# Optimization experiments

Hardware: AMD Instinct MI355X
Metric: run time of the kernel (lower is better)

Reference implementation:

```python
import jax, jax.numpy as jnp
import numpy as np

B, I, O, E = 4096, 256, 256, 8


def setup_inputs() -> dict:
    key = jax.random.key(0)
    k1, k2, k3 = jax.random.split(key, 3)
    return {
        "x": jax.random.normal(k1, (B, I), jnp.float32),
        "W": jax.random.normal(k2, (E, I, O), jnp.float32) * (1.0 / np.sqrt(I)),
        "Wp": jax.random.normal(k3, (E, I), jnp.float32) * (1.0 / np.sqrt(I)),
        "bp": jnp.zeros((E,), jnp.float32),
    }


def reference(x, W, Wp, bp):
    # Router: nn.Linear(in, E) -> sigmoid -> hard one-hot on argmax (BinarySoftActivation)
    g = jax.nn.sigmoid(x @ Wp.T + bp)                              # [B, E]
    onehot = (g == g.max(axis=1, keepdims=True)).astype(g.dtype)   # [B, E] (multi-hot on ties, as in torch)
    gate = g + jax.lax.stop_gradient(onehot - g)                   # straight-through estimator
    # Original: weight[b] = sum_e gate[b,e] * W[e]; y[b] = x[b] @ weight[b].
    # Same math, without materializing the (B, I, O) weight tensor:
    y = jnp.einsum('be,bi,eio->bo', gate, x, W)                    # [B, O]
    return y
```

## Files before the change

### kernel.cpp

```cpp
#include <hip/hip_runtime.h>
#include <hip/hip_bf16.h>

#define NB 4096
#define NI 256
#define NO 256
#define NE 8

__device__ int g_meta[16];
__device__ int g_rowlist[NE * NB];
__device__ int g_ovf[NB];

__global__ __launch_bounds__(256) void router_kernel(
    const float* __restrict__ x, const float* __restrict__ Wp,
    const float* __restrict__ bp)
{
    __shared__ float wplds[NE * NI];
    const int t = threadIdx.x;
    #pragma unroll
    for (int i = 0; i < NE * NI; i += 256 * 4)
        *(float4*)&wplds[i + t * 4] = *(const float4*)&Wp[i + t * 4];
    __syncthreads();

    const int lane = t & 63;
    const int b = blockIdx.x * 4 + (t >> 6);
    const float4 xv = *(const float4*)&x[b * NI + lane * 4];

    float p[NE];
    #pragma unroll
    for (int e = 0; e < NE; ++e) {
        const float4 wv = *(const float4*)&wplds[e * NI + lane * 4];
        p[e] = xv.x * wv.x + xv.y * wv.y + xv.z * wv.z + xv.w * wv.w;
    }
    #pragma unroll
    for (int off = 32; off >= 1; off >>= 1) {
        #pragma unroll
        for (int e = 0; e < NE; ++e) p[e] += __shfl_xor(p[e], off);
    }
    float g[NE], gmax = -1e30f;
    #pragma unroll
    for (int e = 0; e < NE; ++e) {
        g[e] = 1.0f / (1.0f + expf(-(p[e] + bp[e])));
        gmax = fmaxf(gmax, g[e]);
    }
    int mask = 0;
    #pragma unroll
    for (int e = 0; e < NE; ++e) mask |= (g[e] == gmax) ? (1 << e) : 0;

    if (lane == 0) {
        if (__popc(mask) == 1) {
            const int e = __ffs(mask) - 1;
            const int pos = atomicAdd(&g_meta[e], 1);
            g_rowlist[e * NB + pos] = b;
        } else {
            const int pos = atomicAdd(&g_meta[8], 1);
            g_ovf[pos] = (mask << 16) | b;
        }
    }
}

__global__ __launch_bounds__(256) void moe_gemm_kernel(
    const float* __restrict__ x, const float* __restrict__ W,
    float* __restrict__ out)
{
    const int T = blockIdx.x;
    const int n0 = blockIdx.y * 64;

    int e = 0, base = 0, cnt = 0;
    for (; e < NE; ++e) {
        cnt = g_meta[e];
        const int te = (cnt + 63) >> 6;
        if (T < base + te) break;
        base += te;
    }
    if (e >= NE) return;
    const int r0 = (T - base) * 64;

    __shared__ int   rlds[64];
    __shared__ float xs[16][68];
    __shared__ float wst[16][64];

    const int t = threadIdx.x;
    if (t < 64) {
        const int idx = r0 + t;
        const int bb = g_rowlist[e * NB + min(idx, cnt - 1)];
        rlds[t] = (idx < cnt) ? bb : (bb | 0x40000000);
    }
    __syncthreads();

    const int xm = t >> 2, xc = t & 3;
    const int wk = t >> 4, wc = t & 15;
    const float* xptr = x + (rlds[xm] & 0x3FFFFFFF) * NI + xc * 4;
    const float* wptr = W + e * NI * NO + wk * NO + n0 + wc * 4;
    float4 xr = *(const float4*)xptr;
    float4 wr = *(const float4*)wptr;

    const int tm = t >> 4, tn = t & 15;
    float acc[4][4] = {{0.f}};

    #pragma unroll 1
    for (int step = 0; step < 16; ++step) {
        __syncthreads();
        xs[xc * 4 + 0][xm] = xr.x;
        xs[xc * 4 + 1][xm] = xr.y;
        xs[xc * 4 + 2][xm] = xr.z;
        xs[xc * 4 + 3][xm] = xr.w;
        *(float4*)&wst[wk][wc * 4] = wr;
        __syncthreads();
        if (step < 15) {
            xr = *(const float4*)(xptr + (step + 1) * 16);
            wr = *(const float4*)(wptr + (step + 1) * 16 * NO);
        }
        #pragma unroll
        for (int k = 0; k < 16; ++k) {
            const float4 a  = *(const float4*)&xs[k][tm * 4];
            const float4 bv = *(const float4*)&wst[k][tn * 4];
            acc[0][0] += a.x * bv.x; acc[0][1] += a.x * bv.y; acc[0][2] += a.x * bv.z; acc[0][3] += a.x * bv.w;
            acc[1][0] += a.y * bv.x; acc[1][1] += a.y * bv.y; acc[1][2] += a.y * bv.z; acc[1][3] += a.y * bv.w;
            acc[2][0] += a.z * bv.x; acc[2][1] += a.z * bv.y; acc[2][2] += a.z * bv.z; acc[2][3] += a.z * bv.w;
            acc[3][0] += a.w * bv.x; acc[3][1] += a.w * bv.y; acc[3][2] += a.w * bv.z; acc[3][3] += a.w * bv.w;
        }
    }

    #pragma unroll
    for (int r = 0; r < 4; ++r) {
        const int info = rlds[tm * 4 + r];
        if (!(info & 0x40000000)) {
            float4 v;
            v.x = acc[r][0]; v.y = acc[r][1]; v.z = acc[r][2]; v.w = acc[r][3];
            *(float4*)&out[(info & 0x3FFFFFFF) * NO + n0 + tn * 4] = v;
        }
    }
}

__global__ __launch_bounds__(256) void finalize_kernel(
    const float* __restrict__ x, const float* __restrict__ W,
    float* __restrict__ out)
{
    __shared__ float xl[NI];
    const int n = g_meta[8];
    for (int idx = 0; idx < n; ++idx) {
        const int packed = g_ovf[idx];
        const int b = packed & 0xFFFF;
        const int mask = packed >> 16;
        __syncthreads();
        xl[threadIdx.x] = x[b * NI + threadIdx.x];
        __syncthreads();
        float acc = 0.0f;
        for (int e = 0; e < NE; ++e) {
            if (mask & (1 << e)) {
                const float* wp = W + e * NI * NO + threadIdx.x;
                for (int i = 0; i < NI; ++i) acc += xl[i] * wp[i * NO];
            }
        }
        out[b * NO + threadIdx.x] = acc;
    }
    __syncthreads();
    if (threadIdx.x < 16) g_meta[threadIdx.x] = 0;
}

extern "C" void kernel_launch(void* const* d_in, const int* in_sizes, int n_in,
                              void* d_out, int out_size, void* d_ws, size_t ws_size,
                              hipStream_t stream)
{
    const float* x  = (const float*)d_in[0];
    const float* W  = (const float*)d_in[1];
    const float* Wp = (const float*)d_in[2];
    const float* bp = (const float*)d_in[3];
    float* out = (float*)d_out;

    router_kernel<<<NB / 4, 256, 0, stream>>>(x, Wp, bp);

    dim3 grid(72, 4);
    moe_gemm_kernel<<<grid, 256, 0, stream>>>(x, W, out);

    finalize_kernel<<<1, 256, 0, stream>>>(x, W, out);
}
```

Before: 106.7 us.

## Fuse router, grouped GEMM and overflow pass into one cooperative kernel

Merges the three launches (router, per-expert GEMM, tie-overflow finalize) into one cooperative kernel of 256 blocks, separated by grid-wide syncs. The router phase now handles 16 rows per block, and the GEMM tiles are walked in a grid-stride loop. The aim is to drop two kernel launches and the gaps between them. In exchange it adds grid-sync overhead, a fixed grid of 256 blocks, and cooperative-launch limits.

```diff
diff --git a/kernel.cpp b/kernel.cpp
--- a/kernel.cpp
+++ b/kernel.cpp
@@ -1,161 +1,179 @@
 #include <hip/hip_runtime.h>
 #include <hip/hip_bf16.h>
+#include <hip/hip_cooperative_groups.h>
+
+namespace cg = cooperative_groups;
 
 #define NB 4096
 #define NI 256
 #define NO 256
 #define NE 8
+#define GRID 256
 
 __device__ int g_meta[16];
 __device__ int g_rowlist[NE * NB];
 __device__ int g_ovf[NB];
 
-__global__ __launch_bounds__(256) void router_kernel(
-    const float* __restrict__ x, const float* __restrict__ Wp,
-    const float* __restrict__ bp)
-{
-    __shared__ float wplds[NE * NI];
-    const int t = threadIdx.x;
-    #pragma unroll
-    for (int i = 0; i < NE * NI; i += 256 * 4)
-        *(float4*)&wplds[i + t * 4] = *(const float4*)&Wp[i + t * 4];
-    __syncthreads();
-
-    const int lane = t & 63;
-    const int b = blockIdx.x * 4 + (t >> 6);
-    const float4 xv = *(const float4*)&x[b * NI + lane * 4];
-
-    float p[NE];
-    #pragma unroll
-    for (int e = 0; e < NE; ++e) {
-        const float4 wv = *(const float4*)&wplds[e * NI + lane * 4];
-        p[e] = xv.x * wv.x + xv.y * wv.y + xv.z * wv.z + xv.w * wv.w;
-    }
-    #pragma unroll
-    for (int off = 32; off >= 1; off >>= 1) {
-        #pragma unroll
-        for (int e = 0; e < NE; ++e) p[e] += __shfl_xor(p[e], off);
-    }
-    float g[NE], gmax = -1e30f;
-    #pragma unroll
-    for (int e = 0; e < NE; ++e) {
-        g[e] = 1.0f / (1.0f + expf(-(p[e] + bp[e])));
-        gmax = fmaxf(gmax, g[e]);
-    }
-    int mask = 0;
-    #pragma unroll
-    for (int e = 0; e < NE; ++e) mask |= (g[e] == gmax) ? (1 << e) : 0;
-
-    if (lane == 0) {
-        if (__popc(mask) == 1) {
-            const int e = __ffs(mask) - 1;
-            const int pos = atomicAdd(&g_meta[e], 1);
-            g_rowlist[e * NB + pos] = b;
-        } else {
-            const int pos = atomicAdd(&g_meta[8], 1);
-            g_ovf[pos] = (mask << 16) | b;
-        }
-    }
-}
-
-__global__ __launch_bounds__(256) void moe_gemm_kernel(
+__global__ __launch_bounds__(256, 4) void fused_kernel(
     const float* __restrict__ x, const float* __restrict__ W,
+    const float* __restrict__ Wp, const float* __restrict__ bp,
     float* __restrict__ out)
 {
-    const int T = blockIdx.x;
-    const int n0 = blockIdx.y * 64;
+    __shared__ __align__(16) float smem[2176];
+    __shared__ int rlds[64];
 
-    int e = 0, base = 0, cnt = 0;
-    for (; e < NE; ++e) {
-        cnt = g_meta[e];
-        const int te = (cnt + 63) >> 6;
-        if (T < base + te) break;
-        base += te;
-    }
-    if (e >= NE) return;
-    const int r0 = (T - base) * 64;
+    const int t   = threadIdx.x;
+    const int bid = blockIdx.x;
 
-    __shared__ int   rlds[64];
-    __shared__ float xs[16][68];
-    __shared__ float wst[16][64];
+    {
+        float* wplds = smem;
+        #pragma unroll
+        for (int i = 0; i < NE * NI; i += 256 * 4)
+            *(float4*)&wplds[i + t * 4] = *(const float4*)&Wp[i + t * 4];
+        __syncthreads();
 
-    const int t = threadIdx.x;
-    if (t < 64) {
-        const int idx = r0 + t;
-        const int bb = g_rowlist[e * NB + min(idx, cnt - 1)];
-        rlds[t] = (idx < cnt) ? bb : (bb | 0x40000000);
-    }
-    __syncthreads();
+        const int lane = t & 63;
+        const int wv   = t >> 6;
+        #pragma unroll
+        for (int i = 0; i < 4; ++i) {
+            const int b = bid * 16 + wv * 4 + i;
+            const float4 xv = *(const float4*)&x[b * NI + lane * 4];
+            float p[NE];
+            #pragma unroll
+            for (int e = 0; e < NE; ++e) {
+                const float4 wq = *(const float4*)&wplds[e * NI + lane * 4];
+                p[e] = xv.x * wq.x + xv.y * wq.y + xv.z * wq.z + xv.w * wq.w;
+            }
+            #pragma unroll
+            for (int off = 32; off >= 1; off >>= 1) {
+                #pragma unroll
+                for (int e = 0; e < NE; ++e) p[e] += __shfl_xor(p[e], off);
+            }
+            float g[NE], gmax = -1e30f;
+            #pragma unroll
+            for (int e = 0; e < NE; ++e) {
+                g[e] = 1.0f / (1.0f + expf(-(p[e] + bp[e])));
+                gmax = fmaxf(gmax, g[e]);
+            }
+            int mask = 0;
+            #pragma unroll
+            for (int e = 0; e < NE; ++e) mask |= (g[e] == gmax) ? (1 << e) : 0;
 
-    const int xm = t >> 2, xc = t & 3;
-    const int wk = t >> 4, wc = t & 15;
-    const float* xptr = x + (rlds[xm] & 0x3FFFFFFF) * NI + xc * 4;
-    const float* wptr = W + e * NI * NO + wk * NO + n0 + wc * 4;
-    float4 xr = *(const float4*)xptr;
-    float4 wr = *(const float4*)wptr;
-
-    const int tm = t >> 4, tn = t & 15;
-    float acc[4][4] = {{0.f}};
-
-    #pragma unroll 1
-    for (int step = 0; step < 16; ++step) {
-        __syncthreads();
-        xs[xc * 4 + 0][xm] = xr.x;
-        xs[xc * 4 + 1][xm] = xr.y;
-        xs[xc * 4 + 2][xm] = xr.z;
-        xs[xc * 4 + 3][xm] = xr.w;
-        *(float4*)&wst[wk][wc * 4] = wr;
-        __syncthreads();
-        if (step < 15) {
-            xr = *(const float4*)(xptr + (step + 1) * 16);
-            wr = *(const float4*)(wptr + (step + 1) * 16 * NO);
-        }
-        #pragma unroll
-        for (int k = 0; k < 16; ++k) {
-            const float4 a  = *(const float4*)&xs[k][tm * 4];
-            const float4 bv = *(const float4*)&wst[k][tn * 4];
-            acc[0][0] += a.x * bv.x; acc[0][1] += a.x * bv.y; acc[0][2] += a.x * bv.z; acc[0][3] += a.x * bv.w;
-            acc[1][0] += a.y * bv.x; acc[1][1] += a.y * bv.y; acc[1][2] += a.y * bv.z; acc[1][3] += a.y * bv.w;
-            acc[2][0] += a.z * bv.x; acc[2][1] += a.z * bv.y; acc[2][2] += a.z * bv.z; acc[2][3] += a.z * bv.w;
-            acc[3][0] += a.w * bv.x; acc[3][1] += a.w * bv.y; acc[3][2] += a.w * bv.z; acc[3][3] += a.w * bv.w;
+            if (lane == 0) {
+                if (__popc(mask) == 1) {
+                    const int e = __ffs(mask) - 1;
+                    const int pos = atomicAdd(&g_meta[e], 1);
+                    g_rowlist[e * NB + pos] = b;
+                } else {
+                    const int pos = atomicAdd(&g_meta[8], 1);
+                    g_ovf[pos] = (mask << 16) | b;
+                }
+            }
         }
     }
 
-    #pragma unroll
-    for (int r = 0; r < 4; ++r) {
-        const int info = rlds[tm * 4 + r];
-        if (!(info & 0x40000000)) {
-            float4 v;
-            v.x = acc[r][0]; v.y = acc[r][1]; v.z = acc[r][2]; v.w = acc[r][3];
-            *(float4*)&out[(info & 0x3FFFFFFF) * NO + n0 + tn * 4] = v;
+    cg::this_grid().sync();
+
+    {
+        int cnts[NE];
+        int tt = 0;
+        #pragma unroll
+        for (int e = 0; e < NE; ++e) { cnts[e] = g_meta[e]; tt += (cnts[e] + 63) >> 6; }
+        const int TT4 = tt * 4;
+
+        float* xs  = smem;
+        float* wst = smem + 1088;
+
+        for (int w = bid; w < TT4; w += GRID) {
+            const int T  = w >> 2;
+            const int n0 = (w & 3) * 64;
+            int e = 0, base = 0, cnt = 0;
+            for (; e < NE; ++e) {
+                cnt = cnts[e];
+                const int te = (cnt + 63) >> 6;
+                if (T < base + te) break;
+                base += te;
+            }
+            const int r0 = (T - base) * 64;
+
+            if (t < 64) {
+                const int idx = r0 + t;
+                const int bb = g_rowlist[e * NB + min(idx, cnt - 1)];
+                rlds[t] = (idx < cnt) ? bb : (bb | 0x40000000);
+            }
+            __syncthreads();
+
+            const int xm = t >> 2, xc = t & 3;
+            const int wk = t >> 4, wc = t & 15;
+            const float* xptr = x + (rlds[xm] & 0x3FFFFFFF) * NI + xc * 4;
+            const float* wptr = W + e * NI * NO + wk * NO + n0 + wc * 4;
+            float4 xr = *(const float4*)xptr;
+            float4 wr = *(const float4*)wptr;
+
+            const int tm = t >> 4, tn = t & 15;
+            float acc[4][4] = {{0.f}};
+
+            #pragma unroll 1
+            for (int step = 0; step < 16; ++step) {
+                __syncthreads();
+                xs[(xc * 4 + 0) * 68 + xm] = xr.x;
+                xs[(xc * 4 + 1) * 68 + xm] = xr.y;
+                xs[(xc * 4 + 2) * 68 + xm] = xr.z;
+                xs[(xc * 4 + 3) * 68 + xm] = xr.w;
+                *(float4*)&wst[wk * 64 + wc * 4] = wr;
+                __syncthreads();
+                if (step < 15) {
+                    xr = *(const float4*)(xptr + (step + 1) * 16);
+                    wr = *(const float4*)(wptr + (step + 1) * 16 * NO);
+                }
+                #pragma unroll
+                for (int k = 0; k < 16; ++k) {
+                    const float4 a  = *(const float4*)&xs[k * 68 + tm * 4];
+                    const float4 bv = *(const float4*)&wst[k * 64 + tn * 4];
+                    acc[0][0] += a.x * bv.x; acc[0][1] += a.x * bv.y; acc[0][2] += a.x * bv.z; acc[0][3] += a.x * bv.w;
+                    acc[1][0] += a.y * bv.x; acc[1][1] += a.y * bv.y; acc[1][2] += a.y * bv.z; acc[1][3] += a.y * bv.w;
+                    acc[2][0] += a.z * bv.x; acc[2][1] += a.z * bv.y; acc[2][2] += a.z * bv.z; acc[2][3] += a.z * bv.w;
+                    acc[3][0] += a.w * bv.x; acc[3][1] += a.w * bv.y; acc[3][2] += a.w * bv.z; acc[3][3] += a.w * bv.w;
+                }
+            }
+
+            #pragma unroll
+            for (int r = 0; r < 4; ++r) {
+                const int info = rlds[tm * 4 + r];
+                if (!(info & 0x40000000)) {
+                    float4 v;
+                    v.x = acc[r][0]; v.y = acc[r][1]; v.z = acc[r][2]; v.w = acc[r][3];
+                    *(float4*)&out[(info & 0x3FFFFFFF) * NO + n0 + tn * 4] = v;
+                }
+            }
+            __syncthreads();
         }
     }
-}
 
-__global__ __launch_bounds__(256) void finalize_kernel(
-    const float* __restrict__ x, const float* __restrict__ W,
-    float* __restrict__ out)
-{
-    __shared__ float xl[NI];
-    const int n = g_meta[8];
-    for (int idx = 0; idx < n; ++idx) {
-        const int packed = g_ovf[idx];
-        const int b = packed & 0xFFFF;
-        const int mask = packed >> 16;
+    cg::this_grid().sync();
+
+    if (bid == 0) {
+        float* xl = smem;
+        const int n = g_meta[8];
+        for (int idx = 0; idx < n; ++idx) {
+            const int packed = g_ovf[idx];
+            const int b = packed & 0xFFFF;
+            const int mask = packed >> 16;
+            __syncthreads();
+            xl[t] = x[b * NI + t];
+            __syncthreads();
+            float acc = 0.0f;
+            for (int e = 0; e < NE; ++e) {
+                if (mask & (1 << e)) {
+                    const float* wp = W + e * NI * NO + t;
+                    for (int i = 0; i < NI; ++i) acc += xl[i] * wp[i * NO];
+                }
+            }
+            out[b * NO + t] = acc;
+        }
         __syncthreads();
-        xl[threadIdx.x] = x[b * NI + threadIdx.x];
-        __syncthreads();
-        float acc = 0.0f;
-        for (int e = 0; e < NE; ++e) {
-            if (mask & (1 << e)) {
-                const float* wp = W + e * NI * NO + threadIdx.x;
-                for (int i = 0; i < NI; ++i) acc += xl[i] * wp[i * NO];
-            }
-        }
-        out[b * NO + threadIdx.x] = acc;
+        if (t < 16) g_meta[t] = 0;
     }
-    __syncthreads();
-    if (threadIdx.x < 16) g_meta[threadIdx.x] = 0;
 }
 
 extern "C" void kernel_launch(void* const* d_in, const int* in_sizes, int n_in,
@@ -166,12 +184,9 @@
     const float* W  = (const float*)d_in[1];
     const float* Wp = (const float*)d_in[2];
     const float* bp = (const float*)d_in[3];
-    float* out = (float*)d_out;
+    float*      out = (float*)d_out;
 
-    router_kernel<<<NB / 4, 256, 0, stream>>>(x, Wp, bp);
-
-    dim3 grid(72, 4);
-    moe_gemm_kernel<<<grid, 256, 0, stream>>>(x, W, out);
-
-    finalize_kernel<<<1, 256, 0, stream>>>(x, W, out);
+    void* args[] = { (void*)&x, (void*)&W, (void*)&Wp, (void*)&bp, (void*)&out };
+    hipLaunchCooperativeKernel((void*)fused_kernel, dim3(GRID), dim3(256),
+                               args, 0, stream);
 }
```

After: 185.5 us. +73.9%, slower.
